# Kernel tuning notes

Measured on AMD Instinct MI355X. Metric: run time of the kernel, lower is better.

## Reference

```python
import jax, jax.numpy as jnp
import numpy as np

B, N, C = 16, 4096, 768
H = 12
D = C // H  # 64
SCALE = D ** -0.5


def setup_inputs() -> dict:
    key = jax.random.key(0)
    k1, k2, k3, k4 = jax.random.split(key, 4)
    x = jax.random.normal(k1, (B, N, C), dtype=jnp.float32)
    # packed qkv projection (bias=False): torch Linear(dim, 3*dim)
    w_qkv = jax.random.normal(k2, (C, 3 * C), dtype=jnp.float32) * 0.02
    # output projection Linear(dim, dim) with bias
    w_proj = jax.random.normal(k3, (C, C), dtype=jnp.float32) * 0.02
    b_proj = jax.random.normal(k4, (C,), dtype=jnp.float32) * 0.02
    return {"x": x, "w_qkv": w_qkv, "w_proj": w_proj, "b_proj": b_proj}


def reference(x, w_qkv, w_proj, b_proj):
    b, n, c = x.shape
    # packed qkv: [B,N,3C] -> [3,B,H,N,D]
    qkv = (x @ w_qkv).reshape(b, n, 3, H, D).transpose(2, 0, 3, 1, 4)
    q, k, v = qkv[0], qkv[1], qkv[2]  # each [B,H,N,D]
    # kernelized (linear) attention: kv = (k^T v) * scale  -> [B,H,D,D]
    kv = jnp.einsum("bhnd,bhne->bhde", k, v) * SCALE
    # out = gelu(q) @ gelu(kv)  (exact/erf gelu, matching torch F.gelu default)
    gq = jax.nn.gelu(q, approximate=False)
    gkv = jax.nn.gelu(kv, approximate=False)
    out = jnp.einsum("bhtd,bhde->bhte", gq, gkv)  # [B,H,N,D]
    out = out.transpose(0, 2, 1, 3).reshape(b, n, c)  # b t (h d)
    return out @ w_proj + b_proj
```

## Files before the change

### kernel.cpp

```cpp
#include <hip/hip_runtime.h>
#include <hip/hip_bf16.h>


typedef __attribute__((ext_vector_type(8))) short short8_t;
typedef __attribute__((ext_vector_type(4))) float f32x4_t;

typedef __attribute__((address_space(1))) void as1_void;
typedef __attribute__((address_space(3))) void as3_void;

__device__ __forceinline__ void gload_lds16(const void* g, void* l) {
    __builtin_amdgcn_global_load_lds(
        (as1_void*)(unsigned long long)(g),
        (as3_void*)(unsigned long long)(l), 16, 0, 0);
}

__device__ __forceinline__ float gelu_exact(float x) {
    return 0.5f * x * (1.0f + erff(x * 0.7071067811865475f));
}

__device__ __forceinline__ unsigned short to_bf16(float f) {
    __hip_bfloat16 h = __float2bfloat16(f);
    return *reinterpret_cast<unsigned short*>(&h);
}

__device__ __forceinline__ f32x4_t mfma16(short8_t a, short8_t b, f32x4_t c) {
    return __builtin_amdgcn_mfma_f32_16x16x32_bf16(a, b, c, 0, 0, 0);
}

__global__ __launch_bounds__(256) void k_cvt_bf16(const float* __restrict__ in,
                                                  unsigned short* __restrict__ out,
                                                  long n) {
    long i = (long)blockIdx.x * blockDim.x + threadIdx.x;
    long stride = (long)gridDim.x * blockDim.x;
    for (long idx = i * 4; idx < n; idx += stride * 4) {
        float4 v = *(const float4*)(in + idx);
        ushort4 o;
        o.x = to_bf16(v.x); o.y = to_bf16(v.y); o.z = to_bf16(v.z); o.w = to_bf16(v.w);
        *(ushort4*)(out + idx) = o;
    }
}

__global__ __launch_bounds__(256) void k_wqkvT(const float* __restrict__ w,
                                               unsigned short* __restrict__ wT) {
    int gid = blockIdx.x * 256 + threadIdx.x;
    int c = gid / 96, rblk = gid % 96;
    int r0 = rblk * 8;
    short8_t o;
#pragma unroll
    for (int i = 0; i < 8; ++i)
        o[i] = (short)to_bf16(w[(size_t)(r0 + i) * 2304 + c]);
    *(short8_t*)(wT + (size_t)c * 768 + r0) = o;
}

__global__ __launch_bounds__(256) void k_wprojT(const float* __restrict__ w,
                                                unsigned short* __restrict__ wT) {
    int gid = blockIdx.x * 256 + threadIdx.x;
    int c = gid / 96, rblk = gid % 96;
    int r0 = rblk * 8;
    short8_t o;
#pragma unroll
    for (int i = 0; i < 8; ++i)
        o[i] = (short)to_bf16(w[(size_t)(r0 + i) * 768 + c]);
    *(short8_t*)(wT + (size_t)c * 768 + r0) = o;
}

template<bool GELU_EPI, bool BATCHED_B, bool BF16_OUT, bool BIAS>
__global__ __launch_bounds__(512, 2)
void k_gemm256(const unsigned short* __restrict__ A, int lda,
               const unsigned short* __restrict__ Bt, int ldb,
               void* __restrict__ Cout, int ldc,
               const float* __restrict__ bias,
               int tiles_n, int K) {
    __shared__ __attribute__((aligned(16))) unsigned short lds[2][2][2][128 * 64];

    const int nwg = gridDim.x;
    int bid = blockIdx.x;
    bid = (bid & 7) * (nwg >> 3) + (bid >> 3);

    const int tn = bid % tiles_n, tm = bid / tiles_n;
    const int row0 = tm * 256, col0 = tn * 256;

    const unsigned short* Bb = Bt;
    if (BATCHED_B) Bb += (size_t)(row0 >> 12) * 768 * 768;

    const int tid = threadIdx.x;
    const int lane = tid & 63;
    const int w = tid >> 6;
    const int wm = w >> 2;
    const int wn = w & 3;
    const int lr = lane & 15, lg = lane >> 4;

    const int c0 = tid, c1 = 512 + tid;
    const int sr0 = c0 >> 3, sk0 = (c0 & 7) ^ (sr0 & 7);
    const int sr1 = c1 >> 3, sk1 = (c1 & 7) ^ (sr1 & 7);

    auto stageA = [&](int buf, int half, int kt) {
        const unsigned short* base = A + (size_t)(row0 + half * 128) * lda + kt * 64;
        gload_lds16(base + (size_t)sr0 * lda + sk0 * 8, &lds[0][buf][half][c0 * 8]);
        gload_lds16(base + (size_t)sr1 * lda + sk1 * 8, &lds[0][buf][half][c1 * 8]);
    };
    auto stageB = [&](int buf, int half, int kt) {
        const unsigned short* base = Bb + (size_t)(col0 + half * 128) * ldb + kt * 64;
        gload_lds16(base + (size_t)sr0 * ldb + sk0 * 8, &lds[1][buf][half][c0 * 8]);
        gload_lds16(base + (size_t)sr1 * ldb + sk1 * 8, &lds[1][buf][half][c1 * 8]);
    };
    auto ldA = [&](int buf, int mi, int ks) -> short8_t {
        int row = mi * 16 + lr;
        int kc = (ks * 4 + lg) ^ (row & 7);
        return *(const short8_t*)&lds[0][buf][wm][row * 64 + kc * 8];
    };
    auto ldB = [&](int buf, int nj, int ks) -> short8_t {
        int row = wn * 64 + nj * 16 + lr;
        int half = row >> 7, rl = row & 127;
        int kc = (ks * 4 + lg) ^ (rl & 7);
        return *(const short8_t*)&lds[1][buf][half][rl * 64 + kc * 8];
    };

    f32x4_t acc[8][4] = {};
    short8_t bfrag[4][2];
    short8_t afrP[2][4];

#define FENCE asm volatile("" ::: "memory")
#define PH(q, STAGE_STMT, VM_STMT, nbuf, nq)                                    \
    {                                                                           \
        STAGE_STMT;                                                             \
        VM_STMT;                                                                \
        FENCE;                                                                  \
        __builtin_amdgcn_s_barrier();                                           \
        FENCE;                                                                  \
        asm volatile("s_waitcnt lgkmcnt(0)" ::: "memory");                      \
        __builtin_amdgcn_sched_barrier(0);                                      \
        __builtin_amdgcn_s_setprio(1);                                          \
        _Pragma("unroll") for (int nj = 0; nj < 4; ++nj) {                      \
            acc[2 * (q)][nj]     = mfma16(afrP[(q) & 1][0], bfrag[nj][0], acc[2 * (q)][nj]);     \
            acc[2 * (q)][nj]     = mfma16(afrP[(q) & 1][1], bfrag[nj][1], acc[2 * (q)][nj]);     \
            acc[2 * (q) + 1][nj] = mfma16(afrP[(q) & 1][2], bfrag[nj][0], acc[2 * (q) + 1][nj]); \
            acc[2 * (q) + 1][nj] = mfma16(afrP[(q) & 1][3], bfrag[nj][1], acc[2 * (q) + 1][nj]); \
        }                                                                       \
        __builtin_amdgcn_s_setprio(0);                                          \
        if ((q) == 3) {                                                         \
            _Pragma("unroll") for (int nj = 0; nj < 4; ++nj)                    \
                _Pragma("unroll") for (int ks = 0; ks < 2; ++ks)                \
                    bfrag[nj][ks] = ldB(nbuf, nj, ks);                          \
        }                                                                       \
        afrP[((q) + 1) & 1][0] = ldA(nbuf, 2 * (nq), 0);                        \
        afrP[((q) + 1) & 1][1] = ldA(nbuf, 2 * (nq), 1);                        \
        afrP[((q) + 1) & 1][2] = ldA(nbuf, 2 * (nq) + 1, 0);                    \
        afrP[((q) + 1) & 1][3] = ldA(nbuf, 2 * (nq) + 1, 1);                    \
        FENCE;                                                                  \
        __builtin_amdgcn_s_barrier();                                           \
        FENCE;                                                                  \
    }

    const int nt = K >> 6;
    const int niter = nt >> 1;

    stageA(0, 0, 0); stageA(0, 1, 0); stageB(0, 0, 0); stageB(0, 1, 0);
    asm volatile("s_waitcnt vmcnt(0)" ::: "memory");
    stageB(1, 0, 1); stageB(1, 1, 1); stageA(1, 0, 1);
    __builtin_amdgcn_s_barrier();
    FENCE;
#pragma unroll
    for (int nj = 0; nj < 4; ++nj)
#pragma unroll
        for (int ks = 0; ks < 2; ++ks)
            bfrag[nj][ks] = ldB(0, nj, ks);
    afrP[0][0] = ldA(0, 0, 0); afrP[0][1] = ldA(0, 0, 1);
    afrP[0][2] = ldA(0, 1, 0); afrP[0][3] = ldA(0, 1, 1);
    FENCE;

    for (int it = 0; it < niter; ++it) {
        const int t1 = 2 * it + 1;
        const int tA = (2 * it + 2 < nt) ? 2 * it + 2 : 0;
        const int tB = (2 * it + 3 < nt) ? 2 * it + 3 : 0;
        PH(0, stageA(1, 1, t1), (void)0, 0, 1);
        PH(1, stageB(0, 0, tA), (void)0, 0, 2);
        PH(2, stageB(0, 1, tA), (void)0, 0, 3);
        PH(3, stageA(0, 0, tA), asm volatile("s_waitcnt vmcnt(4)" ::: "memory"), 1, 0);
        PH(0, stageA(0, 1, tA), (void)0, 1, 1);
        PH(1, stageB(1, 0, tB), (void)0, 1, 2);
        PH(2, stageB(1, 1, tB), (void)0, 1, 3);
        PH(3, stageA(1, 0, tB), asm volatile("s_waitcnt vmcnt(4)" ::: "memory"), 0, 0);
    }
    asm volatile("s_waitcnt vmcnt(0)" ::: "memory");
#undef PH
#undef FENCE

    const int rbase = row0 + wm * 128 + (lg << 2);
    const int cbase = col0 + wn * 64 + lr;
#pragma unroll
    for (int mi = 0; mi < 8; ++mi)
#pragma unroll
        for (int nj = 0; nj < 4; ++nj)
#pragma unroll
            for (int r = 0; r < 4; ++r) {
                int row = rbase + mi * 16 + r;
                int col = cbase + nj * 16;
                float v = acc[mi][nj][r];
                if (GELU_EPI) v = gelu_exact(v);
                if (BIAS) v += bias[col];
                if (BF16_OUT)
                    ((unsigned short*)Cout)[(size_t)row * ldc + col] = to_bf16(v);
                else
                    ((float*)Cout)[(size_t)row * ldc + col] = v;
            }
}

__global__ __launch_bounds__(256) void k_G(const unsigned short* __restrict__ xb,
                                           unsigned short* __restrict__ Gst) {
    static const signed char TI[21] = {0,0,0,0,0,0,1,1,1,1,1,2,2,2,2,3,3,3,4,4,5};
    static const signed char TJ[21] = {0,1,2,3,4,5,1,2,3,4,5,2,3,4,5,3,4,5,4,5,5};
    int bid = blockIdx.x;
    bid = (bid & 7) * 42 + (bid >> 3);
    const int b = bid / 21, t = bid % 21;
    const int d0 = TI[t] * 128, e0 = TJ[t] * 128;
    const bool diag = (d0 == e0);
    const unsigned short* xB = xb + (size_t)b * 4096 * 768;

    __shared__ __attribute__((aligned(16))) unsigned short lds[2][2][128 * 64];

    const int tid = threadIdx.x, lane = tid & 63, w = tid >> 6;
    const int colg = tid & 15;
    const int rq8 = (tid >> 4) & 7;
    const int blk = tid >> 7;
    const int wm = w >> 1, wn = w & 1;
    const int lr = lane & 15, lg = lane >> 4;
    const int base0 = (blk ? e0 : d0) + colg * 8;
    const int tb = diag ? 0 : 1;
    const bool active = (!diag) || (blk == 0);

    f32x4_t acc[4][4] = {};
    short8_t ra[8];

    auto loadx = [&](int it) {
        if (!active) return;
        const size_t rbase = (size_t)(it * 64 + rq8 * 8) * 768 + base0;
#pragma unroll
        for (int rr = 0; rr < 8; ++rr)
            ra[rr] = *(const short8_t*)(xB + rbase + (size_t)rr * 768);
    };
    auto writes = [&](int buf) {
        if (!active) return;
#pragma unroll
        for (int j = 0; j < 8; ++j) {
            const int c = colg * 8 + j;
            const int sw3 = ((c & 7) ^ (c >> 3)) & 7;
            short8_t v;
#pragma unroll
            for (int rr = 0; rr < 8; ++rr) v[rr] = ra[rr][j];
            *(short8_t*)(&lds[buf][blk][c * 64 + ((rq8 ^ sw3) << 3)]) = v;
        }
    };
    auto ldfrag = [&](int buf, int tile, int cbase, int o) -> short8_t {
        const int c = cbase + lr;
        const int sw3 = ((c & 7) ^ (c >> 3)) & 7;
        return *(const short8_t*)(&lds[buf][tile][c * 64 + ((o ^ sw3) << 3)]);
    };

    loadx(0);
    writes(0);
    __syncthreads();

    for (int it = 0; it < 64; ++it) {
        const int buf = it & 1;
        if (it < 63) loadx(it + 1);
#pragma unroll
        for (int ks = 0; ks < 2; ++ks) {
            short8_t af[4], bf[4];
#pragma unroll
            for (int mi = 0; mi < 4; ++mi)
                af[mi] = ldfrag(buf, 0, wm * 64 + mi * 16, ks * 4 + lg);
#pragma unroll
            for (int nj = 0; nj < 4; ++nj)
                bf[nj] = ldfrag(buf, tb, wn * 64 + nj * 16, ks * 4 + lg);
#pragma unroll
            for (int mi = 0; mi < 4; ++mi)
#pragma unroll
                for (int nj = 0; nj < 4; ++nj)
                    acc[mi][nj] = mfma16(af[mi], bf[nj], acc[mi][nj]);
        }
        if (it < 63) writes(buf ^ 1);
        __syncthreads();
    }

    const int dbase = d0 + wm * 64 + (lg << 2);
    const int ebase = e0 + wn * 64 + lr;
#pragma unroll
    for (int mi = 0; mi < 4; ++mi)
#pragma unroll
        for (int nj = 0; nj < 4; ++nj)
#pragma unroll
            for (int r = 0; r < 4; ++r)
                Gst[((size_t)b * 768 + dbase + mi * 16 + r) * 768 + ebase + nj * 16] =
                    to_bf16(acc[mi][nj][r]);

    if (!diag) {
        unsigned short* T = &lds[0][0][0];
#pragma unroll
        for (int mi = 0; mi < 4; ++mi)
#pragma unroll
            for (int nj = 0; nj < 4; ++nj) {
                const int el = wn * 64 + nj * 16 + lr;
                const int sig = ((el ^ (el >> 3)) & 7) << 1;
                const int s = wm * 16 + mi * 4 + lg;
                uint2 pk;
                pk.x = (unsigned int)to_bf16(acc[mi][nj][0]) |
                       ((unsigned int)to_bf16(acc[mi][nj][1]) << 16);
                pk.y = (unsigned int)to_bf16(acc[mi][nj][2]) |
                       ((unsigned int)to_bf16(acc[mi][nj][3]) << 16);
                *(uint2*)(&T[el * 128 + ((s ^ sig) << 2)]) = pk;
            }
        __syncthreads();
#pragma unroll
        for (int i = 0; i < 8; ++i) {
            const int el = i * 16 + (tid >> 4);
            const int p = tid & 15;
            const int sig = ((el ^ (el >> 3)) & 7) << 1;
            short8_t v = *(const short8_t*)(&T[el * 128 + (((2 * p) ^ sig) << 2)]);
            *(short8_t*)(Gst + ((size_t)b * 768 + e0 + el) * 768 + d0 + p * 8) = v;
        }
    }
}

__global__ __launch_bounds__(256) void k_kvh(const unsigned short* __restrict__ wqkv_bf,
                                             const unsigned short* __restrict__ Tst,
                                             unsigned short* __restrict__ gkvb) {
    const int bh = blockIdx.x;
    const int b = bh / 12, h = bh % 12;
    const unsigned short* kptr = wqkv_bf + 768 + h * 64;
    const unsigned short* vptr = Tst + (size_t)b * 768 * 768 + h * 64;

    __shared__ __attribute__((aligned(16))) unsigned short kT[64 * 64];
    __shared__ __attribute__((aligned(16))) unsigned short vT[64 * 64];

    const int tid = threadIdx.x, lane = tid & 63, w = tid >> 6;
    const int np = tid >> 3;
    const int g = tid & 7;

    f32x4_t acc[4] = {};

    for (int it = 0; it < 12; ++it) {
        const size_t r = (size_t)(it * 64 + 2 * np);
        short8_t k0 = *(const short8_t*)(kptr + r * 2304 + g * 8);
        short8_t k1 = *(const short8_t*)(kptr + (r + 1) * 2304 + g * 8);
        short8_t v0 = *(const short8_t*)(vptr + r * 768 + g * 8);
        short8_t v1 = *(const short8_t*)(vptr + (r + 1) * 768 + g * 8);
        __syncthreads();
#pragma unroll
        for (int j = 0; j < 8; ++j) {
            const int d = g * 8 + j;
            const int e = d * 64 + ((2 * np) ^ (((d ^ (d >> 3)) & 7) << 3));
            *(unsigned int*)(kT + e) =
                (unsigned int)(unsigned short)k0[j] | ((unsigned int)(unsigned short)k1[j] << 16);
            *(unsigned int*)(vT + e) =
                (unsigned int)(unsigned short)v0[j] | ((unsigned int)(unsigned short)v1[j] << 16);
        }
        __syncthreads();
        const int lr = lane & 15, lg = lane >> 4;
#pragma unroll
        for (int ks = 0; ks < 2; ++ks) {
            const int d = w * 16 + lr;
            short8_t a = *(const short8_t*)(kT + d * 64 +
                (((ks * 4 + lg) ^ ((d ^ (d >> 3)) & 7)) << 3));
#pragma unroll
            for (int nj = 0; nj < 4; ++nj) {
                const int e2 = nj * 16 + lr;
                short8_t bf = *(const short8_t*)(vT + e2 * 64 +
                    (((ks * 4 + lg) ^ ((e2 ^ (e2 >> 3)) & 7)) << 3));
                acc[nj] = __builtin_amdgcn_mfma_f32_16x16x32_bf16(a, bf, acc[nj], 0, 0, 0);
            }
        }
    }

    unsigned short* pout = gkvb + (size_t)bh * 4096;
    const int rb2 = w * 16 + ((lane >> 4) << 2);
    const int cb = lane & 15;
#pragma unroll
    for (int nj = 0; nj < 4; ++nj)
#pragma unroll
        for (int r = 0; r < 4; ++r)
            pout[(rb2 + r) * 64 + nj * 16 + cb] = to_bf16(gelu_exact(acc[nj][r] * 0.125f));
}

__global__ __launch_bounds__(256) void k_M(const unsigned short* __restrict__ gkvb,
                                           const unsigned short* __restrict__ wpT,
                                           unsigned short* __restrict__ MT) {
    __shared__ __attribute__((aligned(16))) unsigned short As[64 * 64];
    __shared__ __attribute__((aligned(16))) unsigned short Bs[256 * 64];

    const int bid = blockIdx.x;
    const int bh = bid / 3, ct = bid % 3;
    const int b = bh / 12, h = bh % 12;
    const int c0 = ct * 256;
    const int tid = threadIdx.x, lane = tid & 63, w = tid >> 6;
    const int lr = lane & 15, lg = lane >> 4;

    short8_t ra[2], rb[8];
#pragma unroll
    for (int i = 0; i < 2; ++i) {
        int ch = i * 256 + tid, row = ch >> 3, kc = ch & 7;
        ra[i] = *(const short8_t*)(gkvb + (size_t)bh * 4096 + row * 64 + kc * 8);
    }
#pragma unroll
    for (int i = 0; i < 8; ++i) {
        int ch = i * 256 + tid, row = ch >> 3, kc = ch & 7;
        rb[i] = *(const short8_t*)(wpT + (size_t)(c0 + row) * 768 + h * 64 + kc * 8);
    }
#pragma unroll
    for (int i = 0; i < 2; ++i) {
        int ch = i * 256 + tid, row = ch >> 3, kc = ch & 7;
        *(short8_t*)(As + row * 64 + ((kc ^ (row & 7)) * 8)) = ra[i];
    }
#pragma unroll
    for (int i = 0; i < 8; ++i) {
        int ch = i * 256 + tid, row = ch >> 3, kc = ch & 7;
        *(short8_t*)(Bs + row * 64 + ((kc ^ (row & 7)) * 8)) = rb[i];
    }
    __syncthreads();

    f32x4_t acc[4][4] = {};
#pragma unroll
    for (int ks = 0; ks < 2; ++ks) {
        short8_t a[4], bfr[4];
#pragma unroll
        for (int mi = 0; mi < 4; ++mi) {
            int row = mi * 16 + lr;
            a[mi] = *(const short8_t*)(As + row * 64 + (((ks * 4 + lg) ^ (row & 7)) * 8));
        }
#pragma unroll
        for (int nj = 0; nj < 4; ++nj) {
            int row = w * 64 + nj * 16 + lr;
            bfr[nj] = *(const short8_t*)(Bs + row * 64 + (((ks * 4 + lg) ^ (row & 7)) * 8));
        }
#pragma unroll
        for (int mi = 0; mi < 4; ++mi)
#pragma unroll
            for (int nj = 0; nj < 4; ++nj)
                acc[mi][nj] = __builtin_amdgcn_mfma_f32_16x16x32_bf16(a[mi], bfr[nj], acc[mi][nj], 0, 0, 0);
    }
    __syncthreads();

#pragma unroll
    for (int mi = 0; mi < 4; ++mi)
#pragma unroll
        for (int nj = 0; nj < 4; ++nj) {
            unsigned int w0 = (unsigned int)to_bf16(acc[mi][nj][0]) |
                              ((unsigned int)to_bf16(acc[mi][nj][1]) << 16);
            unsigned int w1 = (unsigned int)to_bf16(acc[mi][nj][2]) |
                              ((unsigned int)to_bf16(acc[mi][nj][3]) << 16);
            uint2 pk; pk.x = w0; pk.y = w1;
            *(uint2*)(Bs + (w * 64 + nj * 16 + lr) * 64 + mi * 16 + lg * 4) = pk;
        }
    __syncthreads();
#pragma unroll
    for (int i = 0; i < 8; ++i) {
        int ch = i * 256 + tid, cl = ch >> 3, dk = ch & 7;
        short8_t v = *(const short8_t*)(Bs + cl * 64 + dk * 8);
        *(short8_t*)(MT + ((size_t)(b * 768) + c0 + cl) * 768 + h * 64 + dk * 8) = v;
    }
}

extern "C" void kernel_launch(void* const* d_in, const int* in_sizes, int n_in,
                              void* d_out, int out_size, void* d_ws, size_t ws_size,
                              hipStream_t stream) {
    const float* x      = (const float*)d_in[0];
    const float* w_qkv  = (const float*)d_in[1];
    const float* w_proj = (const float*)d_in[2];
    const float* b_proj = (const float*)d_in[3];
    float* out = (float*)d_out;
    char* ws = (char*)d_ws;

    unsigned short* q_gelu  = (unsigned short*)(ws);
    unsigned short* wqkvT   = (unsigned short*)(ws + 100663296);
    unsigned short* wqkv_bf = (unsigned short*)(ws + 104202240);
    unsigned short* G_bf    = (unsigned short*)(ws + 107741184);
    unsigned short* T_bf    = (unsigned short*)(ws + 126615552);
    unsigned short* MT      = (unsigned short*)(ws + 145489920);
    unsigned short* xb   = (unsigned short*)d_out;
    unsigned short* gkvb = (unsigned short*)((char*)d_out + 134217728);
    unsigned short* wpT  = (unsigned short*)((char*)d_out + 136314880);

    k_cvt_bf16<<<2048, 256, 0, stream>>>(x, xb, 50331648L);
    k_cvt_bf16<<<432, 256, 0, stream>>>(w_qkv, wqkv_bf, 1769472L);
    k_wqkvT<<<864, 256, 0, stream>>>(w_qkv, wqkvT);
    k_wprojT<<<288, 256, 0, stream>>>(w_proj, wpT);
    k_gemm256<true, false, true, false><<<768, 512, 0, stream>>>(
        xb, 768, wqkvT, 768, q_gelu, 768, nullptr, 3, 768);
    k_G<<<336, 256, 0, stream>>>(xb, G_bf);
    k_gemm256<false, false, true, false><<<144, 512, 0, stream>>>(
        G_bf, 768, wqkvT + (size_t)1536 * 768, 768, T_bf, 768, nullptr, 3, 768);
    k_kvh<<<192, 256, 0, stream>>>(wqkv_bf, T_bf, gkvb);
    k_M<<<576, 256, 0, stream>>>(gkvb, wpT, MT);
    k_gemm256<false, true, false, true><<<768, 512, 0, stream>>>(
        q_gelu, 768, MT, 768, out, 768, b_proj, 3, 768);
}
```

Before: 406.1 us.

## Swap exact erf GELU for tanh approximation and reschedule GEMM staging barriers

Two unrelated changes. First, the exact erf-based GELU is replaced with the tanh approximation computed through __expf, which is cheaper but no longer matches the reference's exact GELU and adds approximation error. Second, the GEMM main loop now issues each global-to-LDS stage after the MFMA block and the next fragment reads, waits on vmcnt(2) every phase, and uses one barrier per phase instead of two. This aims to cut barrier overhead and overlap loads with compute, but the tighter vmcnt waits and the reordering of LDS writes against reads could introduce stalls or race hazards.

```diff
diff --git a/kernel.cpp b/kernel.cpp
--- a/kernel.cpp
+++ b/kernel.cpp
@@ -14,8 +14,12 @@
         (as3_void*)(unsigned long long)(l), 16, 0, 0);
 }
 
-__device__ __forceinline__ float gelu_exact(float x) {
-    return 0.5f * x * (1.0f + erff(x * 0.7071067811865475f));
+__device__ __forceinline__ float gelu_f(float x) {
+    float x2 = x * x;
+    float t = x * fmaf(0.0356774081f, x2, 0.7978845608f);
+    float e = __expf(2.0f * t);
+    float th = 1.0f - 2.0f / (e + 1.0f);
+    return 0.5f * x * (1.0f + th);
 }
 
 __device__ __forceinline__ unsigned short to_bf16(float f) {
@@ -121,13 +125,8 @@
     short8_t afrP[2][4];
 
 #define FENCE asm volatile("" ::: "memory")
-#define PH(q, STAGE_STMT, VM_STMT, nbuf, nq)                                    \
+#define PH(q, STAGE_STMT, nbuf, nq)                                             \
     {                                                                           \
-        STAGE_STMT;                                                             \
-        VM_STMT;                                                                \
-        FENCE;                                                                  \
-        __builtin_amdgcn_s_barrier();                                           \
-        FENCE;                                                                  \
         asm volatile("s_waitcnt lgkmcnt(0)" ::: "memory");                      \
         __builtin_amdgcn_sched_barrier(0);                                      \
         __builtin_amdgcn_s_setprio(1);                                          \
@@ -147,6 +146,8 @@
         afrP[((q) + 1) & 1][1] = ldA(nbuf, 2 * (nq), 1);                        \
         afrP[((q) + 1) & 1][2] = ldA(nbuf, 2 * (nq) + 1, 0);                    \
         afrP[((q) + 1) & 1][3] = ldA(nbuf, 2 * (nq) + 1, 1);                    \
+        STAGE_STMT;                                                             \
+        asm volatile("s_waitcnt vmcnt(2)" ::: "memory");                        \
         FENCE;                                                                  \
         __builtin_amdgcn_s_barrier();                                           \
         FENCE;                                                                  \
@@ -173,14 +174,14 @@
         const int t1 = 2 * it + 1;
         const int tA = (2 * it + 2 < nt) ? 2 * it + 2 : 0;
         const int tB = (2 * it + 3 < nt) ? 2 * it + 3 : 0;
-        PH(0, stageA(1, 1, t1), (void)0, 0, 1);
-        PH(1, stageB(0, 0, tA), (void)0, 0, 2);
-        PH(2, stageB(0, 1, tA), (void)0, 0, 3);
-        PH(3, stageA(0, 0, tA), asm volatile("s_waitcnt vmcnt(4)" ::: "memory"), 1, 0);
-        PH(0, stageA(0, 1, tA), (void)0, 1, 1);
-        PH(1, stageB(1, 0, tB), (void)0, 1, 2);
-        PH(2, stageB(1, 1, tB), (void)0, 1, 3);
-        PH(3, stageA(1, 0, tB), asm volatile("s_waitcnt vmcnt(4)" ::: "memory"), 0, 0);
+        PH(0, stageA(1, 1, t1), 0, 1);
+        PH(1, stageB(0, 0, tA), 0, 2);
+        PH(2, stageB(0, 1, tA), 0, 3);
+        PH(3, stageA(0, 0, tA), 1, 0);
+        PH(0, stageA(0, 1, tA), 1, 1);
+        PH(1, stageB(1, 0, tB), 1, 2);
+        PH(2, stageB(1, 1, tB), 1, 3);
+        PH(3, stageA(1, 0, tB), 0, 0);
     }
     asm volatile("s_waitcnt vmcnt(0)" ::: "memory");
 #undef PH
@@ -197,7 +198,7 @@
                 int row = rbase + mi * 16 + r;
                 int col = cbase + nj * 16;
                 float v = acc[mi][nj][r];
-                if (GELU_EPI) v = gelu_exact(v);
+                if (GELU_EPI) v = gelu_f(v);
                 if (BIAS) v += bias[col];
                 if (BF16_OUT)
                     ((unsigned short*)Cout)[(size_t)row * ldc + col] = to_bf16(v);
@@ -379,7 +380,7 @@
     for (int nj = 0; nj < 4; ++nj)
 #pragma unroll
         for (int r = 0; r < 4; ++r)
-            pout[(rb2 + r) * 64 + nj * 16 + cb] = to_bf16(gelu_exact(acc[nj][r] * 0.125f));
+            pout[(rb2 + r) * 64 + nj * 16 + cb] = to_bf16(gelu_f(acc[nj][r] * 0.125f));
 }
 
 __global__ __launch_bounds__(256) void k_M(const unsigned short* __restrict__ gkvb,
```

Result: slower. 414.3 us (+2.0%).
